# Optimization experiments

Measured on AMD Instinct MI355X. Metric: run time of the kernel, lower is better.

The kernel has to match this reference:

```python
import jax, jax.numpy as jnp
import numpy as np

# Fixed 16-node graph hardcoded in the torch module (src row, dst row)
_SRC = np.array([0,0,0,0,1,1,2,2,3,4,4,4,4,5,5,5,6,6,7,8,8,8,8,9,9,10,10,11,12,12,12,13,13,14,14,15])
_DST = np.array([1,4,5,8,0,2,1,3,2,0,5,8,12,0,4,6,5,7,6,0,4,9,12,8,10,9,11,10,4,8,13,12,14,13,15,14])
_N = 16

def _gcn_adj():
    # PyG GCNConv default: add self-loops, symmetric normalization D^-1/2 (A+I) D^-1/2
    A = np.zeros((_N, _N), dtype=np.float32)
    A[_DST, _SRC] = 1.0  # messages flow src -> dst
    A = A + np.eye(_N, dtype=np.float32)
    deg = A.sum(axis=1)
    dinv = 1.0 / np.sqrt(deg)
    return jnp.asarray(dinv[:, None] * A * dinv[None, :])  # [16,16]

_AHAT = _gcn_adj()


def setup_inputs() -> dict:
    key = jax.random.key(0)
    ks = jax.random.split(key, 9)
    B, F = 65536, 64
    def rn(k, shape, scale=0.05):
        return jax.random.normal(k, shape, dtype=jnp.float32) * scale
    return {
        "obs": jax.random.normal(ks[0], (B, _N, F), dtype=jnp.float32),
        "W1": rn(ks[1], (F, 64)),   "b1": rn(ks[2], (64,)),
        "W2": rn(ks[3], (64, 128)), "b2": rn(ks[4], (128,)),
        "W3": rn(ks[5], (128, 256)),"b3": rn(ks[6], (256,)),
        "Wfc": rn(ks[7], (256, 256)),"bfc": rn(ks[8], (256,)),
    }


def _gcn_layer(x, W, b):
    # x: [B,16,Fin] -> A_hat @ (x W) + b : [B,16,Fout]
    h = jnp.einsum("bnf,fg->bng", x, W)
    return jnp.einsum("mn,bng->bmg", _AHAT, h) + b


def reference(obs, W1, b1, W2, b2, W3, b3, Wfc, bfc):
    x = jax.nn.elu(_gcn_layer(obs, W1, b1))
    x = jax.nn.elu(_gcn_layer(x, W2, b2))
    x = jax.nn.elu(_gcn_layer(x, W3, b3))
    x = jnp.max(x, axis=1)              # MaxAggregation over the 16 nodes -> [B,256]
    x = jax.nn.elu(x @ Wfc + bfc)       # fc + elu
    return x
```

## Files before the change

kernel.cpp:

```cpp
#include <hip/hip_runtime.h>
#include <hip/hip_bf16.h>

typedef __bf16 bf16x8 __attribute__((ext_vector_type(8)));
typedef __bf16 bf16x4 __attribute__((ext_vector_type(4)));
typedef float  f32x4  __attribute__((ext_vector_type(4)));
typedef unsigned short u16;

#define S_TILE 8
#define ROWS   128
#define XT_STRIDE 136
#define Z_STRIDE  136
#define P_STRIDE  264

__device__ const u16   g_adj[16] = {0x0133,0x0007,0x000E,0x000C,0x1131,0x0071,0x00E0,0x00C0,
                                    0x1311,0x0700,0x0E00,0x0C00,0x3110,0x7000,0xE000,0xC000};
__device__ const float g_deg[16] = {5,3,3,2,5,4,3,2,5,3,3,2,4,3,3,2};

__device__ __forceinline__ float elu_f(float x) {
    return x > 0.0f ? x : (__expf(x) - 1.0f);
}

__global__ void prepack_kernel(const float* __restrict__ W1, const float* __restrict__ W2,
                               const float* __restrict__ W3, const float* __restrict__ Wfc,
                               __bf16* __restrict__ out)
{
    int t = blockIdx.x * blockDim.x + threadIdx.x;
    const float* W; int N; long obase;
    if      (t < 512)   { W = W1;  N = 64;  obase = 0;     }
    else if (t < 1536)  { W = W2;  N = 128; obase = 4096;  t -= 512;  }
    else if (t < 5632)  { W = W3;  N = 256; obase = 12288; t -= 1536; }
    else if (t < 13824) { W = Wfc; N = 256; obase = 45056; t -= 5632; }
    else return;
    const int frag = t >> 6;
    const int lane = t & 63;
    const int NT = N / 16;
    const int kt = frag / NT;
    const int nt = frag % NT;
    const int n  = nt * 16 + (lane & 15);
    const int k0 = kt * 32 + (lane >> 4) * 8;
    #pragma unroll
    for (int j = 0; j < 8; ++j)
        out[obase + ((long)frag * 64 + lane) * 8 + j] = (__bf16)W[(long)(k0 + j) * N + n];
}

template<int FIN, int FOUT, bool LAST>
__device__ __forceinline__ void gcn_layer(u16* sXT, u16* sZ, u16* sPool,
                                          const __bf16* __restrict__ Wp,
                                          const float* __restrict__ bias,
                                          bf16x8 ahat, int lane, int wv)
{
    const int col = lane & 15;
    const int g   = lane >> 4;

    constexpr int FBW = (FIN / 16) / 4;
    #pragma unroll
    for (int fbi = 0; fbi < FBW; ++fbi) {
        const int fb = wv * FBW + fbi;
        const u16* xbase = &sXT[(fb * 16 + col) * XT_STRIDE + (g & 1) * 8];
        #pragma unroll
        for (int s = 0; s < S_TILE; ++s) {
            bf16x8 a = *reinterpret_cast<const bf16x8*>(xbase + s * 16);
            f32x4 c = {0.f, 0.f, 0.f, 0.f};
            c = __builtin_amdgcn_mfma_f32_16x16x32_bf16(a, ahat, c, 0, 0, 0);
            bf16x4 zp;
            #pragma unroll
            for (int i = 0; i < 4; ++i) zp[i] = (__bf16)c[i];
            *reinterpret_cast<bf16x4*>(&sZ[(s * 16 + col) * Z_STRIDE + fb * 16 + g * 4]) = zp;
        }
    }
    __syncthreads();

    constexpr int NT  = FOUT / 16;
    constexpr int KT  = FIN / 32;
    constexpr int NBW = NT / 4;
    #pragma unroll
    for (int nbi = 0; nbi < NBW; ++nbi) {
        const int nb = wv * NBW + nbi;
        bf16x8 bfr[KT];
        #pragma unroll
        for (int kt = 0; kt < KT; ++kt)
            bfr[kt] = *reinterpret_cast<const bf16x8*>(Wp + ((long)(kt * NT + nb) * 64 + lane) * 8);
        const float bv = bias[nb * 16 + col];
        #pragma unroll
        for (int s = 0; s < S_TILE; ++s) {
            f32x4 acc = {0.f, 0.f, 0.f, 0.f};
            #pragma unroll
            for (int kt = 0; kt < KT; ++kt) {
                bf16x8 a = *reinterpret_cast<const bf16x8*>(
                    &sZ[(s * 16 + col) * Z_STRIDE + kt * 32 + g * 8]);
                acc = __builtin_amdgcn_mfma_f32_16x16x32_bf16(a, bfr[kt], acc, 0, 0, 0);
            }
            if (!LAST) {
                bf16x4 xp;
                #pragma unroll
                for (int i = 0; i < 4; ++i) xp[i] = (__bf16)elu_f(acc[i] + bv);
                *reinterpret_cast<bf16x4*>(&sXT[(nb * 16 + col) * XT_STRIDE + s * 16 + g * 4]) = xp;
            } else {
                float m = fmaxf(fmaxf(acc[0], acc[1]), fmaxf(acc[2], acc[3]));
                m = fmaxf(m, __shfl_xor(m, 16));
                m = fmaxf(m, __shfl_xor(m, 32));
                m = elu_f(m + bv);
                if (g == 0) {
                    __bf16 h = (__bf16)m;
                    sPool[s * P_STRIDE + nb * 16 + col] = __builtin_bit_cast(u16, h);
                }
            }
        }
    }
    __syncthreads();
}

__global__ __launch_bounds__(256, 2) void gcn_fused(
    const float* __restrict__ obs,
    const float* __restrict__ b1, const float* __restrict__ b2,
    const float* __restrict__ b3, const float* __restrict__ bfc,
    const __bf16* __restrict__ Wp, float* __restrict__ out)
{
    __shared__ u16 sXT[128 * XT_STRIDE];
    __shared__ u16 sZ[ROWS * Z_STRIDE];
    __shared__ u16 sPool[16 * P_STRIDE];

    const int tid  = threadIdx.x;
    const int lane = tid & 63;
    const int wv   = tid >> 6;
    const int col  = lane & 15;
    const int g    = lane >> 4;

    bf16x8 ahat;
    #pragma unroll
    for (int j = 0; j < 8; ++j) {
        const int k = g * 8 + j;
        float v = 0.f;
        if (k < 16 && ((g_adj[col] >> k) & 1)) v = rsqrtf(g_deg[col] * g_deg[k]);
        ahat[j] = (__bf16)v;
    }

    const long rowBase = (long)blockIdx.x * ROWS;
    const float* obs_t = obs + rowBase * 64;
    {
        const int q  = tid & 15;
        const int r0 = (tid >> 4) * 8;
        float vals[4][8];
        #pragma unroll
        for (int i = 0; i < 8; ++i) {
            const float4 v = reinterpret_cast<const float4*>(obs_t)[(r0 + i) * 16 + q];
            vals[0][i] = v.x; vals[1][i] = v.y; vals[2][i] = v.z; vals[3][i] = v.w;
        }
        #pragma unroll
        for (int f = 0; f < 4; ++f) {
            bf16x8 p;
            #pragma unroll
            for (int i = 0; i < 8; ++i) p[i] = (__bf16)vals[f][i];
            *reinterpret_cast<bf16x8*>(&sXT[(q * 4 + f) * XT_STRIDE + r0]) = p;
        }
    }
    __syncthreads();

    gcn_layer< 64,  64, false>(sXT, sZ, sPool, Wp + 0,     b1, ahat, lane, wv);
    gcn_layer< 64, 128, false>(sXT, sZ, sPool, Wp + 4096,  b2, ahat, lane, wv);
    gcn_layer<128, 256, true >(sXT, sZ, sPool, Wp + 12288, b3, ahat, lane, wv);

    const __bf16* Wf = Wp + 45056;
    bf16x8 afc[8];
    #pragma unroll
    for (int kt = 0; kt < 8; ++kt)
        afc[kt] = *reinterpret_cast<const bf16x8*>(&sPool[col * P_STRIDE + kt * 32 + g * 8]);
    const long sampleBase = (long)blockIdx.x * S_TILE;
    #pragma unroll
    for (int nbi = 0; nbi < 4; ++nbi) {
        const int nb = wv * 4 + nbi;
        f32x4 acc = {0.f, 0.f, 0.f, 0.f};
        #pragma unroll
        for (int kt = 0; kt < 8; ++kt) {
            bf16x8 b = *reinterpret_cast<const bf16x8*>(Wf + ((long)(kt * 16 + nb) * 64 + lane) * 8);
            acc = __builtin_amdgcn_mfma_f32_16x16x32_bf16(afc[kt], b, acc, 0, 0, 0);
        }
        const float bv = bfc[nb * 16 + col];
        if (g < 2) {
            #pragma unroll
            for (int i = 0; i < 4; ++i)
                out[(sampleBase + g * 4 + i) * 256 + nb * 16 + col] = elu_f(acc[i] + bv);
        }
    }
}

extern "C" void kernel_launch(void* const* d_in, const int* in_sizes, int n_in,
                              void* d_out, int out_size, void* d_ws, size_t ws_size,
                              hipStream_t stream) {
    const float* obs = (const float*)d_in[0];
    const float* W1  = (const float*)d_in[1];
    const float* b1  = (const float*)d_in[2];
    const float* W2  = (const float*)d_in[3];
    const float* b2  = (const float*)d_in[4];
    const float* W3  = (const float*)d_in[5];
    const float* b3  = (const float*)d_in[6];
    const float* Wfc = (const float*)d_in[7];
    const float* bfc = (const float*)d_in[8];
    __bf16* Wp = (__bf16*)d_ws;
    float* out = (float*)d_out;

    const int B = in_sizes[0] / (16 * 64);
    prepack_kernel<<<dim3(54), dim3(256), 0, stream>>>(W1, W2, W3, Wfc, Wp);
    gcn_fused<<<dim3(B / S_TILE), dim3(256), 0, stream>>>(obs, b1, b2, b3, bfc, Wp, out);
}
```

Baseline: 575.0 us.

## Halve sample tile, XOR-swizzle LDS layouts, hoist A fragments, raise occupancy

Reduces the per-block sample tile from 8 to 4 so LDS per block shrinks, and raises launch bounds to 4 blocks per SM to improve latency hiding. The padded LDS strides are replaced with XOR-swizzled 8-element groups to avoid bank conflicts. The A fragments of the second GEMM are loaded once into registers per layer instead of being reloaded for each output block. In exchange, the fc stage now wastes three quarters of each MFMA, the weight fragments are fetched from global memory twice as often per sample, and register pressure from the hoisted fragments may cause spills under the tighter launch bound.

```diff
diff --git a/kernel.cpp b/kernel.cpp
--- a/kernel.cpp
+++ b/kernel.cpp
@@ -6,11 +6,10 @@
 typedef float  f32x4  __attribute__((ext_vector_type(4)));
 typedef unsigned short u16;
 
-#define S_TILE 8
-#define ROWS   128
-#define XT_STRIDE 136
-#define Z_STRIDE  136
-#define P_STRIDE  264
+#define S_TILE 4
+#define ROWS   64
+#define P_STRIDE 264
+
 
 __device__ const u16   g_adj[16] = {0x0133,0x0007,0x000E,0x000C,0x1131,0x0071,0x00E0,0x00C0,
                                     0x1311,0x0700,0x0E00,0x0C00,0x3110,0x7000,0xE000,0xC000};
@@ -51,21 +50,25 @@
 {
     const int col = lane & 15;
     const int g   = lane >> 4;
+    const int c7  = col & 7;
 
     constexpr int FBW = (FIN / 16) / 4;
     #pragma unroll
     for (int fbi = 0; fbi < FBW; ++fbi) {
         const int fb = wv * FBW + fbi;
-        const u16* xbase = &sXT[(fb * 16 + col) * XT_STRIDE + (g & 1) * 8];
+        const int f  = fb * 16 + col;
         #pragma unroll
         for (int s = 0; s < S_TILE; ++s) {
-            bf16x8 a = *reinterpret_cast<const bf16x8*>(xbase + s * 16);
+            const int gr = ((s * 2 + (g & 1)) ^ c7);
+            bf16x8 a = *reinterpret_cast<const bf16x8*>(&sXT[f * 64 + gr * 8]);
             f32x4 c = {0.f, 0.f, 0.f, 0.f};
             c = __builtin_amdgcn_mfma_f32_16x16x32_bf16(a, ahat, c, 0, 0, 0);
+            const int r   = s * 16 + col;
+            const int zgr = ((fb * 2 + (g >> 1)) ^ c7);
             bf16x4 zp;
             #pragma unroll
             for (int i = 0; i < 4; ++i) zp[i] = (__bf16)c[i];
-            *reinterpret_cast<bf16x4*>(&sZ[(s * 16 + col) * Z_STRIDE + fb * 16 + g * 4]) = zp;
+            *reinterpret_cast<bf16x4*>(&sZ[r * 128 + zgr * 8 + (g & 1) * 4]) = zp;
         }
     }
     __syncthreads();
@@ -73,6 +76,16 @@
     constexpr int NT  = FOUT / 16;
     constexpr int KT  = FIN / 32;
     constexpr int NBW = NT / 4;
+    bf16x8 afr[S_TILE][KT];
+    #pragma unroll
+    for (int s = 0; s < S_TILE; ++s) {
+        const int r = s * 16 + col;
+        #pragma unroll
+        for (int kt = 0; kt < KT; ++kt) {
+            const int gr = ((kt * 4 + g) ^ c7);
+            afr[s][kt] = *reinterpret_cast<const bf16x8*>(&sZ[r * 128 + gr * 8]);
+        }
+    }
     #pragma unroll
     for (int nbi = 0; nbi < NBW; ++nbi) {
         const int nb = wv * NBW + nbi;
@@ -85,16 +98,15 @@
         for (int s = 0; s < S_TILE; ++s) {
             f32x4 acc = {0.f, 0.f, 0.f, 0.f};
             #pragma unroll
-            for (int kt = 0; kt < KT; ++kt) {
-                bf16x8 a = *reinterpret_cast<const bf16x8*>(
-                    &sZ[(s * 16 + col) * Z_STRIDE + kt * 32 + g * 8]);
-                acc = __builtin_amdgcn_mfma_f32_16x16x32_bf16(a, bfr[kt], acc, 0, 0, 0);
-            }
+            for (int kt = 0; kt < KT; ++kt)
+                acc = __builtin_amdgcn_mfma_f32_16x16x32_bf16(afr[s][kt], bfr[kt], acc, 0, 0, 0);
             if (!LAST) {
+                const int f   = nb * 16 + col;
+                const int xgr = ((s * 2 + (g >> 1)) ^ c7);
                 bf16x4 xp;
                 #pragma unroll
                 for (int i = 0; i < 4; ++i) xp[i] = (__bf16)elu_f(acc[i] + bv);
-                *reinterpret_cast<bf16x4*>(&sXT[(nb * 16 + col) * XT_STRIDE + s * 16 + g * 4]) = xp;
+                *reinterpret_cast<bf16x4*>(&sXT[f * 64 + xgr * 8 + (g & 1) * 4]) = xp;
             } else {
                 float m = fmaxf(fmaxf(acc[0], acc[1]), fmaxf(acc[2], acc[3]));
                 m = fmaxf(m, __shfl_xor(m, 16));
@@ -110,15 +122,15 @@
     __syncthreads();
 }
 
-__global__ __launch_bounds__(256, 2) void gcn_fused(
+__global__ __launch_bounds__(256, 4) void gcn_fused(
     const float* __restrict__ obs,
     const float* __restrict__ b1, const float* __restrict__ b2,
     const float* __restrict__ b3, const float* __restrict__ bfc,
     const __bf16* __restrict__ Wp, float* __restrict__ out)
 {
-    __shared__ u16 sXT[128 * XT_STRIDE];
-    __shared__ u16 sZ[ROWS * Z_STRIDE];
-    __shared__ u16 sPool[16 * P_STRIDE];
+    __shared__ u16 sXT[128 * 64];
+    __shared__ u16 sZ[ROWS * 128];
+    __shared__ u16 sPool[S_TILE * P_STRIDE];
 
     const int tid  = threadIdx.x;
     const int lane = tid & 63;
@@ -138,20 +150,24 @@
     const long rowBase = (long)blockIdx.x * ROWS;
     const float* obs_t = obs + rowBase * 64;
     {
-        const int q  = tid & 15;
-        const int r0 = (tid >> 4) * 8;
-        float vals[4][8];
-        #pragma unroll
-        for (int i = 0; i < 8; ++i) {
+        const int q   = tid & 15;
+        const int rg  = (tid >> 4) & 7;
+        const int dup = tid >> 7;
+        const int r0  = rg * 8 + dup * 4;
+        float vals[4][4];
+        #pragma unroll
+        for (int i = 0; i < 4; ++i) {
             const float4 v = reinterpret_cast<const float4*>(obs_t)[(r0 + i) * 16 + q];
             vals[0][i] = v.x; vals[1][i] = v.y; vals[2][i] = v.z; vals[3][i] = v.w;
         }
         #pragma unroll
         for (int f = 0; f < 4; ++f) {
-            bf16x8 p;
-            #pragma unroll
-            for (int i = 0; i < 8; ++i) p[i] = (__bf16)vals[f][i];
-            *reinterpret_cast<bf16x8*>(&sXT[(q * 4 + f) * XT_STRIDE + r0]) = p;
+            const int feat = q * 4 + f;
+            const int gr   = rg ^ (feat & 7);
+            bf16x4 p;
+            #pragma unroll
+            for (int i = 0; i < 4; ++i) p[i] = (__bf16)vals[f][i];
+            *reinterpret_cast<bf16x4*>(&sXT[feat * 64 + gr * 8 + dup * 4]) = p;
         }
     }
     __syncthreads();
@@ -164,7 +180,7 @@
     bf16x8 afc[8];
     #pragma unroll
     for (int kt = 0; kt < 8; ++kt)
-        afc[kt] = *reinterpret_cast<const bf16x8*>(&sPool[col * P_STRIDE + kt * 32 + g * 8]);
+        afc[kt] = *reinterpret_cast<const bf16x8*>(&sPool[(col & 3) * P_STRIDE + kt * 32 + g * 8]);
     const long sampleBase = (long)blockIdx.x * S_TILE;
     #pragma unroll
     for (int nbi = 0; nbi < 4; ++nbi) {
@@ -176,10 +192,10 @@
             acc = __builtin_amdgcn_mfma_f32_16x16x32_bf16(afc[kt], b, acc, 0, 0, 0);
         }
         const float bv = bfc[nb * 16 + col];
-        if (g < 2) {
+        if (g == 0) {
             #pragma unroll
             for (int i = 0; i < 4; ++i)
-                out[(sampleBase + g * 4 + i) * 256 + nb * 16 + col] = elu_f(acc[i] + bv);
+                out[(sampleBase + i) * 256 + nb * 16 + col] = elu_f(acc[i] + bv);
         }
     }
 }
```

New measurement: 553.4 us. 3.8% less time.
